# Performance work log

Hardware: AMD Instinct MI355X
Metric: run time of the kernel (lower is better)

Reference implementation:

```python
import jax, jax.numpy as jnp
from jax import lax
import numpy as np

BINS = 25
K = 5  # entropy patch size
EPS = 1e-5


def conv2d(x, w, b, stride, pad):
    y = lax.conv_general_dilated(x, w, (stride, stride), [(pad, pad), (pad, pad)],
                                 dimension_numbers=("NCHW", "OIHW", "NCHW"))
    return y + b[None, :, None, None]


def group_norm_per_channel(x, w, b):
    # GroupNorm with num_groups == num_channels: per-channel norm over H,W (biased var)
    mu = x.mean(axis=(2, 3), keepdims=True)
    v = x.var(axis=(2, 3), keepdims=True)
    return (x - mu) / jnp.sqrt(v + EPS) * w[None, :, None, None] + b[None, :, None, None]


def channel_entropy(x):
    # x: (b,c,h,w). Unfold into 5x5 patches, per-patch histc(bins=25) over patch
    # values using that patch's min/max range (torch.histc default), then entropy.
    b, c, h, w = x.shape
    ho, wo = h - K + 1, w - K + 1
    # (b,c,K*K,L) -- fixed 25-position loop, vectorized over all data dims
    patches = jnp.stack([x[:, :, i:i + ho, j:j + wo]
                         for i in range(K) for j in range(K)], axis=2)
    patches = patches.reshape(b, c, K * K, ho * wo)
    mn = patches.min(axis=2, keepdims=True)
    mx = patches.max(axis=2, keepdims=True)
    rng = jnp.where(mx > mn, mx - mn, jnp.ones_like(mx))
    bins = jnp.clip(jnp.floor((patches - mn) / rng * BINS), 0, BINS - 1).astype(jnp.int32)
    # histogram via comparison one-hot: (b,c,L,BINS)
    counts = (bins[..., None] == jnp.arange(BINS, dtype=jnp.int32)).sum(axis=2)
    pk = counts.astype(x.dtype) / (K * K)
    ent = (-pk * jnp.log(jnp.clip(pk, 1e-5, 1.0 - 1e-5))).sum(axis=-1).mean(axis=-1)  # (b,c)
    return ent[:, :, None, None]


def instance_norm_ent(x, w, b):
    ent = channel_entropy(lax.stop_gradient(x))
    mu = x.mean(axis=(2, 3), keepdims=True)
    n = x.shape[2] * x.shape[3]
    v = x.var(axis=(2, 3), keepdims=True) * (n / (n - 1))  # unbiased var (torch default)
    return (x - mu) / jnp.sqrt(v + EPS) * w[None, :, None, None] * ent + b[None, :, None, None]


def setup_inputs() -> dict:
    key = jax.random.key(0)
    ks = jax.random.split(key, 24)
    s = 0.05
    d = {
        "x": jax.random.normal(ks[0], (64, 3, 224, 224), jnp.float32),
        "conv0_w": jax.random.normal(ks[1], (8, 3, 7, 7), jnp.float32) * s,
        "conv0_b": jax.random.normal(ks[2], (8,), jnp.float32) * s,
        "conv1_w": jax.random.normal(ks[3], (16, 8, 5, 5), jnp.float32) * s,
        "conv1_b": jax.random.normal(ks[4], (16,), jnp.float32) * s,
        "conv2_w": jax.random.normal(ks[5], (32, 16, 3, 3), jnp.float32) * s,
        "conv2_b": jax.random.normal(ks[6], (32,), jnp.float32) * s,
        "gn0_w": jnp.ones((8,), jnp.float32) + jax.random.normal(ks[7], (8,), jnp.float32) * s,
        "gn0_b": jax.random.normal(ks[8], (8,), jnp.float32) * s,
        "n1_w": jnp.ones((16,), jnp.float32) + jax.random.normal(ks[9], (16,), jnp.float32) * s,
        "n1_b": jax.random.normal(ks[10], (16,), jnp.float32) * s,
        "n2_w": jnp.ones((32,), jnp.float32) + jax.random.normal(ks[11], (32,), jnp.float32) * s,
        "n2_b": jax.random.normal(ks[12], (32,), jnp.float32) * s,
        "bn_g": jnp.ones((10368,), jnp.float32) + jax.random.normal(ks[13], (10368,), jnp.float32) * s,
        "bn_b": jax.random.normal(ks[14], (10368,), jnp.float32) * s,
        "fc1_w": jax.random.normal(ks[15], (32, 10368), jnp.float32) * 0.01,
        "fc1_b": jax.random.normal(ks[16], (32,), jnp.float32) * s,
        "shape_w": jax.random.normal(ks[17], (5, 32), jnp.float32) * s,
        "shape_b": jax.random.normal(ks[18], (5,), jnp.float32) * s,
        "vern_w": jax.random.normal(ks[19], (2, 32), jnp.float32) * s,
        "vern_b": jax.random.normal(ks[20], (2,), jnp.float32) * s,
    }
    return d


def reference(x, conv0_w, conv0_b, conv1_w, conv1_b, conv2_w, conv2_b,
              gn0_w, gn0_b, n1_w, n1_b, n2_w, n2_b,
              bn_g, bn_b, fc1_w, fc1_b, shape_w, shape_b, vern_w, vern_b):
    h = conv2d(x, conv0_w, conv0_b, 4, 2)          # (b,8,56,56)
    h = jax.nn.relu(group_norm_per_channel(h, gn0_w, gn0_b))
    h = conv2d(h, conv1_w, conv1_b, 3, 1)          # (b,16,18,18)
    h = jax.nn.relu(instance_norm_ent(h, n1_w, n1_b))
    h = conv2d(h, conv2_w, conv2_b, 1, 1)          # (b,32,18,18)
    h = jax.nn.relu(instance_norm_ent(h, n2_w, n2_b))
    h = h.reshape(h.shape[0], -1)                  # (b,10368)
    # BatchNorm1d (training mode: batch stats, biased var)
    mu = h.mean(axis=0)
    v = h.var(axis=0)
    h = (h - mu) / jnp.sqrt(v + EPS) * bn_g + bn_b
    h = jax.nn.relu(h @ fc1_w.T + fc1_b)           # (b,32)
    out_shape = jax.nn.softmax(h @ shape_w.T + shape_b, axis=-1)
    out_vern = jax.nn.softmax(h @ vern_w.T + vern_b, axis=-1)
    return (out_shape, out_vern)
```

## Files before the change

### kernel.cpp

```cpp
#include <hip/hip_runtime.h>
#include <math.h>

#define EPSD 1e-5


__device__ __forceinline__ double waveReduceSumD(double v) {
#pragma unroll
    for (int off = 32; off > 0; off >>= 1)
        v += __shfl_down(v, off, 64);
    return v;
}

template <int NW>
__device__ __forceinline__ double blockReduceSumD(double v, double* buf) {
    int lane = threadIdx.x & 63;
    int w = threadIdx.x >> 6;
    v = waveReduceSumD(v);
    __syncthreads();
    if (lane == 0) buf[w] = v;
    __syncthreads();
    double tot = 0.0;
#pragma unroll
    for (int i = 0; i < NW; i++) tot += buf[i];
    return tot;
}

__device__ __forceinline__ void build_ent_tab(float* tab) {
    int t = threadIdx.x;
    if (t < 26) {
        if (t == 0) tab[0] = 0.f;
        else {
            double pk = (double)t / 25.0;
            double cl = fmin(fmax(pk, 1e-5), 1.0 - 1e-5);
            tab[t] = (float)(-pk * log(cl));
        }
    }
}

__device__ __forceinline__ float patch_ent(const float* ch, int py, int px, const float* tab) {
    float pv[25];
#pragma unroll
    for (int i = 0; i < 5; i++)
#pragma unroll
        for (int j = 0; j < 5; j++)
            pv[i * 5 + j] = ch[(py + i) * 18 + px + j];
    float mn = pv[0], mx = pv[0];
#pragma unroll
    for (int k = 1; k < 25; k++) { mn = fminf(mn, pv[k]); mx = fmaxf(mx, pv[k]); }
    float rng = (mx > mn) ? (mx - mn) : 1.0f;
    unsigned long long a0 = 0ull, a1 = 0ull;
    int a2 = 0;
#pragma unroll
    for (int k = 0; k < 25; k++) {
        float tt = (pv[k] - mn) / rng * 25.0f;
        int bi = (int)floorf(tt);
        bi = bi < 0 ? 0 : (bi > 24 ? 24 : bi);
        unsigned sh0 = ((unsigned)(5 * bi)) & 63u;
        unsigned sh1 = ((unsigned)(5 * bi - 60)) & 63u;
        a0 += (bi < 12) ? (1ull << sh0) : 0ull;
        a1 += (bi >= 12 && bi < 24) ? (1ull << sh1) : 0ull;
        a2 += (bi == 24) ? 1 : 0;
    }
    float ent = 0.f;
#pragma unroll
    for (int k = 0; k < 12; k++) ent += tab[(a0 >> (5 * k)) & 31ull];
#pragma unroll
    for (int k = 0; k < 12; k++) ent += tab[(a1 >> (5 * k)) & 31ull];
    ent += tab[a2];
    return ent;
}

__global__ __launch_bounds__(256, 4) void k_conv0(const float* __restrict__ x,
                                                  const float* __restrict__ w,
                                                  const float* __restrict__ bias,
                                                  float* __restrict__ h0raw,
                                                  double* __restrict__ part0) {
    __shared__ float wsh[1176];
    __shared__ double redbuf[4][16];
    int tile = blockIdx.x;
    int b = blockIdx.y;
    int t = threadIdx.x;
    for (int i = t; i < 1176; i += 256) {
        int tap = i >> 3, c = i & 7;
        wsh[i] = w[c * 147 + tap];
    }
    __syncthreads();
    const float* xb = x + (size_t)b * 150528;
    float acc[8];
    if (t < 224) {
        int oy = tile * 4 + (t / 56);
        int ox = t % 56;
        int y0 = oy * 4 - 2, x0 = ox * 4 - 2;
#pragma unroll
        for (int c = 0; c < 8; c++) acc[c] = bias[c];
        if (y0 >= 0 && y0 + 6 < 224 && x0 >= 0 && x0 + 6 < 224) {
#pragma unroll 1
            for (int ci = 0; ci < 3; ci++) {
                const float* xp = xb + ci * 50176 + y0 * 224 + x0;
#pragma unroll
                for (int ky = 0; ky < 7; ky++) {
#pragma unroll
                    for (int kx = 0; kx < 7; kx++) {
                        float v = xp[ky * 224 + kx];
                        const float4* wv = (const float4*)&wsh[(ci * 49 + ky * 7 + kx) << 3];
                        float4 wa = wv[0], wb = wv[1];
                        acc[0] += v * wa.x; acc[1] += v * wa.y;
                        acc[2] += v * wa.z; acc[3] += v * wa.w;
                        acc[4] += v * wb.x; acc[5] += v * wb.y;
                        acc[6] += v * wb.z; acc[7] += v * wb.w;
                    }
                }
            }
        } else {
            int ky0 = y0 < 0 ? -y0 : 0;
            int ky1 = (224 - y0) < 7 ? (224 - y0) : 7;
            int kx0 = x0 < 0 ? -x0 : 0;
            int kx1 = (224 - x0) < 7 ? (224 - x0) : 7;
#pragma unroll 1
            for (int ci = 0; ci < 3; ci++) {
                const float* xp = xb + ci * 50176;
                for (int ky = ky0; ky < ky1; ky++) {
                    const float* row = xp + (y0 + ky) * 224 + x0;
                    for (int kx = kx0; kx < kx1; kx++) {
                        float v = row[kx];
                        const float4* wv = (const float4*)&wsh[(ci * 49 + ky * 7 + kx) << 3];
                        float4 wa = wv[0], wb = wv[1];
                        acc[0] += v * wa.x; acc[1] += v * wa.y;
                        acc[2] += v * wa.z; acc[3] += v * wa.w;
                        acc[4] += v * wb.x; acc[5] += v * wb.y;
                        acc[6] += v * wb.z; acc[7] += v * wb.w;
                    }
                }
            }
        }
        int opix = oy * 56 + ox;
#pragma unroll
        for (int c = 0; c < 8; c++)
            h0raw[((size_t)b * 8 + c) * 3136 + opix] = acc[c];
    } else {
#pragma unroll
        for (int c = 0; c < 8; c++) acc[c] = 0.f;
    }
    int wv = t >> 6, lane = t & 63;
#pragma unroll
    for (int c = 0; c < 8; c++) {
        double rs = waveReduceSumD((double)acc[c]);
        double rq = waveReduceSumD((double)acc[c] * (double)acc[c]);
        if (lane == 0) { redbuf[wv][c * 2] = rs; redbuf[wv][c * 2 + 1] = rq; }
    }
    __syncthreads();
    if (t < 16) {
        double tot = redbuf[0][t] + redbuf[1][t] + redbuf[2][t] + redbuf[3][t];
        part0[(((size_t)b * 14 + tile) << 4) + t] = tot;
    }
}

__global__ __launch_bounds__(1024) void k_conv1_ent(const float* __restrict__ h0raw,
                                                    const double* __restrict__ part0,
                                                    const float* __restrict__ gw,
                                                    const float* __restrict__ gb,
                                                    const float* __restrict__ w,
                                                    const float* __restrict__ bias,
                                                    const float* __restrict__ nw,
                                                    const float* __restrict__ nb,
                                                    float* __restrict__ h1) {
    __shared__ float xin[25088];
    __shared__ float wsh[800];
    __shared__ float vals[1296];
    __shared__ float tab[26];
    __shared__ float gnp[16];
    __shared__ double redbuf[16][2];
    __shared__ double entbuf[16];
    __shared__ float prm[4][3];
    int b = blockIdx.x >> 2;
    int grp = blockIdx.x & 3;
    int t = threadIdx.x;
    if (t < 8) {
        double s = 0.0, s2 = 0.0;
        const double* p = part0 + ((size_t)b * 14) * 16;
        for (int tile = 0; tile < 14; tile++) {
            s += p[tile * 16 + t * 2];
            s2 += p[tile * 16 + t * 2 + 1];
        }
        double mean = s / 3136.0;
        double var = s2 / 3136.0 - mean * mean;
        double rstd = 1.0 / sqrt(var + EPSD);
        double sc = (double)gw[t] * rstd;
        gnp[t] = (float)sc;
        gnp[8 + t] = (float)((double)gb[t] - mean * sc);
    }
    for (int i = t; i < 800; i += 1024) wsh[i] = w[grp * 800 + i];
    build_ent_tab(tab);
    __syncthreads();
    for (int i = t; i < 25088; i += 1024) {
        int ci = i / 3136;
        xin[i] = fmaxf(h0raw[(size_t)b * 25088 + i] * gnp[ci] + gnp[8 + ci], 0.f);
    }
    __syncthreads();

    int wv = t >> 6, lane = t & 63;
    int c = wv >> 2;
    int q = wv & 3;
    const float* wp0 = wsh + c * 200;
    float* vch = vals + c * 324;
    float bv = bias[grp * 4 + c];
    double s = 0.0, s2 = 0.0;
    for (int p = q * 81 + lane; p < q * 81 + 81; p += 64) {
        int oy = p / 18, ox = p % 18;
        int y0 = oy * 3 - 1, x0 = ox * 3 - 1;
        float acc = bv;
        if (oy >= 1 && ox >= 1) {
#pragma unroll 1
            for (int ci = 0; ci < 8; ci++) {
                const float* xp = xin + ci * 3136 + y0 * 56 + x0;
                const float* wp = wp0 + ci * 25;
#pragma unroll
                for (int ky = 0; ky < 5; ky++)
#pragma unroll
                    for (int kx = 0; kx < 5; kx++)
                        acc += xp[ky * 56 + kx] * wp[ky * 5 + kx];
            }
        } else {
            int ky0 = y0 < 0 ? 1 : 0;
            int kx0 = x0 < 0 ? 1 : 0;
            for (int ci = 0; ci < 8; ci++) {
                const float* xp = xin + ci * 3136;
                const float* wp = wp0 + ci * 25;
                for (int ky = ky0; ky < 5; ky++) {
                    const float* row = xp + (y0 + ky) * 56 + x0;
                    for (int kx = kx0; kx < 5; kx++)
                        acc += row[kx] * wp[ky * 5 + kx];
                }
            }
        }
        vch[p] = acc;
        s += (double)acc; s2 += (double)acc * (double)acc;
    }
    s = waveReduceSumD(s);
    s2 = waveReduceSumD(s2);
    if (lane == 0) { redbuf[wv][0] = s; redbuf[wv][1] = s2; }
    __syncthreads();
    double ent = 0.0;
    if (lane < 49) {
        int pi = q * 49 + lane;
        ent = (double)patch_ent(vch, pi / 14, pi % 14, tab);
    }
    ent = waveReduceSumD(ent);
    if (lane == 0) entbuf[wv] = ent;
    __syncthreads();
    if (t < 4) {
        double ss = 0.0, qq = 0.0, ee = 0.0;
        for (int k = 0; k < 4; k++) {
            ss += redbuf[t * 4 + k][0];
            qq += redbuf[t * 4 + k][1];
            ee += entbuf[t * 4 + k];
        }
        double entmean = ee / 196.0;
        double mean = ss / 324.0;
        double varb = qq / 324.0 - mean * mean;
        double varu = varb * (324.0 / 323.0);
        double rstd = 1.0 / sqrt(varu + EPSD);
        prm[t][0] = (float)mean;
        prm[t][1] = (float)((double)nw[grp * 4 + t] * entmean * rstd);
        prm[t][2] = nb[grp * 4 + t];
    }
    __syncthreads();
    float* outp = h1 + ((size_t)b * 16 + grp * 4) * 324;
    for (int i = t; i < 1296; i += 1024) {
        int cc = i / 324;
        outp[i] = fmaxf((vals[i] - prm[cc][0]) * prm[cc][1] + prm[cc][2], 0.f);
    }
}

__global__ __launch_bounds__(256) void k_conv2_ent(const float* __restrict__ in,
                                                   const float* __restrict__ w,
                                                   const float* __restrict__ bias,
                                                   const float* __restrict__ nw,
                                                   const float* __restrict__ nb,
                                                   float* __restrict__ out) {
    __shared__ float xin[5184];
    __shared__ float vals[324];
    __shared__ float wsh[144];
    __shared__ float tab[26];
    __shared__ double rbuf[4];
    int b = blockIdx.x >> 5;
    int c = blockIdx.x & 31;
    int t = threadIdx.x;
    const float* xb = in + (size_t)b * 5184;
    for (int i = t; i < 5184; i += 256) xin[i] = xb[i];
    for (int i = t; i < 144; i += 256) wsh[i] = w[c * 144 + i];
    build_ent_tab(tab);
    __syncthreads();
    float bv = bias[c];
    double s = 0.0, s2 = 0.0;
    {
        int oy = 1 + (t >> 4), ox = 1 + (t & 15);
        const float* base = xin + (oy - 1) * 18 + (ox - 1);
        float acc = bv;
        for (int ci = 0; ci < 16; ci++) {
            const float* xp = base + ci * 324;
            const float* wp = wsh + ci * 9;
#pragma unroll
            for (int ky = 0; ky < 3; ky++)
#pragma unroll
                for (int kx = 0; kx < 3; kx++)
                    acc += xp[ky * 18 + kx] * wp[ky * 3 + kx];
        }
        vals[oy * 18 + ox] = acc;
        s += (double)acc; s2 += (double)acc * (double)acc;
    }
    if (t < 68) {
        int oy, ox;
        if (t < 18)      { oy = 0;      ox = t; }
        else if (t < 36) { oy = 17;     ox = t - 18; }
        else if (t < 52) { oy = t - 35; ox = 0; }
        else             { oy = t - 51; ox = 17; }
        int y0 = oy - 1, x0 = ox - 1;
        int ky0 = y0 < 0 ? 1 : 0;
        int ky1 = (18 - y0) < 3 ? 2 : 3;
        int kx0 = x0 < 0 ? 1 : 0;
        int kx1 = (18 - x0) < 3 ? 2 : 3;
        float acc = bv;
        for (int ci = 0; ci < 16; ci++) {
            const float* xp = xin + ci * 324;
            const float* wp = wsh + ci * 9;
            for (int ky = ky0; ky < ky1; ky++) {
                const float* row = xp + (y0 + ky) * 18 + x0;
                for (int kx = kx0; kx < kx1; kx++)
                    acc += row[kx] * wp[ky * 3 + kx];
            }
        }
        vals[oy * 18 + ox] = acc;
        s += (double)acc; s2 += (double)acc * (double)acc;
    }
    __syncthreads();
    double ent = 0.0;
    if (t < 196) ent = (double)patch_ent(vals, t / 14, t % 14, tab);
    double entmean = blockReduceSumD<4>(ent, rbuf) / 196.0;
    double ssum  = blockReduceSumD<4>(s, rbuf);
    double s2sum = blockReduceSumD<4>(s2, rbuf);
    double mean = ssum / 324.0;
    double varb = s2sum / 324.0 - mean * mean;
    double varu = varb * (324.0 / 323.0);
    double rstd = 1.0 / sqrt(varu + EPSD);
    float sc = (float)((double)nw[c] * entmean * rstd);
    float mu = (float)mean;
    float be = nb[c];
    float* outp = out + ((size_t)b * 32 + c) * 324;
    for (int idx = t; idx < 324; idx += 256)
        outp[idx] = fmaxf((vals[idx] - mu) * sc + be, 0.f);
}

__global__ __launch_bounds__(256) void k_bnstats(const float* __restrict__ h2,
                                                 const float* __restrict__ g,
                                                 const float* __restrict__ bb,
                                                 float* __restrict__ scale,
                                                 float* __restrict__ shift) {
    int f = blockIdx.x * 256 + threadIdx.x;
    if (f >= 10368) return;
    double s = 0.0, s2 = 0.0;
    for (int b = 0; b < 64; b++) {
        double v = (double)h2[(size_t)b * 10368 + f];
        s += v; s2 += v * v;
    }
    double mean = s / 64.0;
    double var = s2 / 64.0 - mean * mean;
    double rstd = 1.0 / sqrt(var + EPSD);
    double sc = (double)g[f] * rstd;
    scale[f] = (float)sc;
    shift[f] = (float)((double)bb[f] - mean * sc);
}

__global__ __launch_bounds__(256) void k_fc1(const float* __restrict__ h2,
                                             const float* __restrict__ scale,
                                             const float* __restrict__ shift,
                                             const float* __restrict__ w1,
                                             const float* __restrict__ b1,
                                             float* __restrict__ fcout) {
    __shared__ double rbuf[4];
    int b = blockIdx.x >> 5;
    int j = blockIdx.x & 31;
    const float* hb = h2 + (size_t)b * 10368;
    const float* wj = w1 + (size_t)j * 10368;
    double acc = 0.0;
    for (int f = threadIdx.x; f < 10368; f += 256)
        acc += (double)((hb[f] * scale[f] + shift[f]) * wj[f]);
    acc = blockReduceSumD<4>(acc, rbuf);
    if (threadIdx.x == 0)
        fcout[b * 32 + j] = (float)fmax(acc + (double)b1[j], 0.0);
}

__global__ __launch_bounds__(64) void k_heads(const float* __restrict__ fc,
                                              const float* __restrict__ sw,
                                              const float* __restrict__ sb,
                                              const float* __restrict__ vw,
                                              const float* __restrict__ vb,
                                              float* __restrict__ out) {
    int b = threadIdx.x;
    double h[32];
#pragma unroll
    for (int i = 0; i < 32; i++) h[i] = (double)fc[b * 32 + i];
    double lg[5];
    double mx = -1e300;
#pragma unroll
    for (int k = 0; k < 5; k++) {
        double a = (double)sb[k];
#pragma unroll
        for (int i = 0; i < 32; i++) a += h[i] * (double)sw[k * 32 + i];
        lg[k] = a;
        mx = fmax(mx, a);
    }
    double se = 0.0;
#pragma unroll
    for (int k = 0; k < 5; k++) { lg[k] = exp(lg[k] - mx); se += lg[k]; }
#pragma unroll
    for (int k = 0; k < 5; k++) out[b * 5 + k] = (float)(lg[k] / se);
    double l0 = (double)vb[0], l1 = (double)vb[1];
#pragma unroll
    for (int i = 0; i < 32; i++) { l0 += h[i] * (double)vw[i]; l1 += h[i] * (double)vw[32 + i]; }
    double m = fmax(l0, l1);
    double e0 = exp(l0 - m), e1 = exp(l1 - m);
    double inv = 1.0 / (e0 + e1);
    out[320 + b * 2 + 0] = (float)(e0 * inv);
    out[320 + b * 2 + 1] = (float)(e1 * inv);
}

extern "C" void kernel_launch(void* const* d_in, const int* in_sizes, int n_in,
                              void* d_out, int out_size, void* d_ws, size_t ws_size,
                              hipStream_t stream) {
    const float* x       = (const float*)d_in[0];
    const float* conv0_w = (const float*)d_in[1];
    const float* conv0_b = (const float*)d_in[2];
    const float* conv1_w = (const float*)d_in[3];
    const float* conv1_b = (const float*)d_in[4];
    const float* conv2_w = (const float*)d_in[5];
    const float* conv2_b = (const float*)d_in[6];
    const float* gn0_w   = (const float*)d_in[7];
    const float* gn0_b   = (const float*)d_in[8];
    const float* n1_w    = (const float*)d_in[9];
    const float* n1_b    = (const float*)d_in[10];
    const float* n2_w    = (const float*)d_in[11];
    const float* n2_b    = (const float*)d_in[12];
    const float* bn_g    = (const float*)d_in[13];
    const float* bn_b    = (const float*)d_in[14];
    const float* fc1_w   = (const float*)d_in[15];
    const float* fc1_b   = (const float*)d_in[16];
    const float* shape_w = (const float*)d_in[17];
    const float* shape_b = (const float*)d_in[18];
    const float* vern_w  = (const float*)d_in[19];
    const float* vern_b  = (const float*)d_in[20];
    float* out = (float*)d_out;

    double* part0 = (double*)d_ws;
    float* fbase   = (float*)(part0 + 14336);
    float* h0raw   = fbase;
    float* h1      = h0raw + 1605632;
    float* h2      = h1 + 331776;
    float* bnscale = h2 + 663552;
    float* bnshift = bnscale + 10368;
    float* fc      = bnshift + 10368;

    k_conv0<<<dim3(14, 64), dim3(256), 0, stream>>>(x, conv0_w, conv0_b, h0raw, part0);
    k_conv1_ent<<<dim3(256), dim3(1024), 0, stream>>>(h0raw, part0, gn0_w, gn0_b,
                                                      conv1_w, conv1_b, n1_w, n1_b, h1);
    k_conv2_ent<<<dim3(2048), dim3(256), 0, stream>>>(h1, conv2_w, conv2_b, n2_w, n2_b, h2);
    k_bnstats<<<dim3(41), dim3(256), 0, stream>>>(h2, bn_g, bn_b, bnscale, bnshift);
    k_fc1<<<dim3(2048), dim3(256), 0, stream>>>(h2, bnscale, bnshift, fc1_w, fc1_b, fc);
    k_heads<<<dim3(1), dim3(64), 0, stream>>>(fc, shape_w, shape_b, vern_w, vern_b, out);
}
```

Before: 258.0 us.

## Stage conv0 input in phase-split LDS tile, read weights as uniform scalars, split bnstats

conv0 now loads a zero-padded 19-row input tile into shared memory with float4 global loads, de-interleaved by x mod 4 so stride-4 taps read contiguous LDS. Its weights come straight from global memory at wave-uniform addresses so they can go through scalar loads. conv1 interleaves channel pairs in LDS for float2 reads and likewise drops the weight staging, and conv2 reads its weights from global memory. bnstats splits the batch reduction over four waves across 162 blocks to use more CUs. The costs are more LDS per conv0 block, lower declared occupancy, and reliance on the compiler emitting scalar weight loads.

```diff
diff --git a/kernel.cpp b/kernel.cpp
--- a/kernel.cpp
+++ b/kernel.cpp
@@ -70,76 +70,61 @@
     return ent;
 }
 
-__global__ __launch_bounds__(256, 4) void k_conv0(const float* __restrict__ x,
+__global__ __launch_bounds__(256, 3) void k_conv0(const float* __restrict__ x,
                                                   const float* __restrict__ w,
                                                   const float* __restrict__ bias,
                                                   float* __restrict__ h0raw,
                                                   double* __restrict__ part0) {
-    __shared__ float wsh[1176];
+    __shared__ float tile[12996];
     __shared__ double redbuf[4][16];
-    int tile = blockIdx.x;
+    int tl = blockIdx.x;
     int b = blockIdx.y;
     int t = threadIdx.x;
-    for (int i = t; i < 1176; i += 256) {
-        int tap = i >> 3, c = i & 7;
-        wsh[i] = w[c * 147 + tap];
-    }
-    __syncthreads();
+    for (int i = t; i < 12996; i += 256) tile[i] = 0.f;
+    __syncthreads();
+    int y_base = tl * 16 - 2;
     const float* xb = x + (size_t)b * 150528;
+    for (int i = t; i < 3192; i += 256) {
+        int rowid = i / 56, f4 = i % 56;
+        int ci = rowid / 19, r = rowid % 19;
+        int yIn = y_base + r;
+        if (yIn >= 0 && yIn < 224) {
+            float4 v = *(const float4*)&xb[ci * 50176 + yIn * 224 + f4 * 4];
+            float* tp = tile + ci * 4332 + r * 228;
+            tp[114 + f4] = v.x;
+            tp[171 + f4] = v.y;
+            tp[f4 + 1]   = v.z;
+            tp[58 + f4]  = v.w;
+        }
+    }
+    __syncthreads();
     float acc[8];
+#pragma unroll
+    for (int c = 0; c < 8; c++) acc[c] = 0.f;
     if (t < 224) {
-        int oy = tile * 4 + (t / 56);
+        int ry = t / 56;
         int ox = t % 56;
-        int y0 = oy * 4 - 2, x0 = ox * 4 - 2;
 #pragma unroll
         for (int c = 0; c < 8; c++) acc[c] = bias[c];
-        if (y0 >= 0 && y0 + 6 < 224 && x0 >= 0 && x0 + 6 < 224) {
-#pragma unroll 1
-            for (int ci = 0; ci < 3; ci++) {
-                const float* xp = xb + ci * 50176 + y0 * 224 + x0;
-#pragma unroll
-                for (int ky = 0; ky < 7; ky++) {
-#pragma unroll
-                    for (int kx = 0; kx < 7; kx++) {
-                        float v = xp[ky * 224 + kx];
-                        const float4* wv = (const float4*)&wsh[(ci * 49 + ky * 7 + kx) << 3];
-                        float4 wa = wv[0], wb = wv[1];
-                        acc[0] += v * wa.x; acc[1] += v * wa.y;
-                        acc[2] += v * wa.z; acc[3] += v * wa.w;
-                        acc[4] += v * wb.x; acc[5] += v * wb.y;
-                        acc[6] += v * wb.z; acc[7] += v * wb.w;
-                    }
+#pragma unroll
+        for (int ci = 0; ci < 3; ci++) {
+#pragma unroll
+            for (int ky = 0; ky < 7; ky++) {
+                const float* rp = tile + ci * 4332 + (4 * ry + ky) * 228;
+#pragma unroll
+                for (int kx = 0; kx < 7; kx++) {
+                    float v = rp[(kx & 3) * 57 + ox + (kx >> 2)];
+#pragma unroll
+                    for (int c = 0; c < 8; c++)
+                        acc[c] += v * w[c * 147 + ci * 49 + ky * 7 + kx];
                 }
             }
-        } else {
-            int ky0 = y0 < 0 ? -y0 : 0;
-            int ky1 = (224 - y0) < 7 ? (224 - y0) : 7;
-            int kx0 = x0 < 0 ? -x0 : 0;
-            int kx1 = (224 - x0) < 7 ? (224 - x0) : 7;
-#pragma unroll 1
-            for (int ci = 0; ci < 3; ci++) {
-                const float* xp = xb + ci * 50176;
-                for (int ky = ky0; ky < ky1; ky++) {
-                    const float* row = xp + (y0 + ky) * 224 + x0;
-                    for (int kx = kx0; kx < kx1; kx++) {
-                        float v = row[kx];
-                        const float4* wv = (const float4*)&wsh[(ci * 49 + ky * 7 + kx) << 3];
-                        float4 wa = wv[0], wb = wv[1];
-                        acc[0] += v * wa.x; acc[1] += v * wa.y;
-                        acc[2] += v * wa.z; acc[3] += v * wa.w;
-                        acc[4] += v * wb.x; acc[5] += v * wb.y;
-                        acc[6] += v * wb.z; acc[7] += v * wb.w;
-                    }
-                }
-            }
-        }
+        }
+        int oy = tl * 4 + ry;
         int opix = oy * 56 + ox;
 #pragma unroll
         for (int c = 0; c < 8; c++)
             h0raw[((size_t)b * 8 + c) * 3136 + opix] = acc[c];
-    } else {
-#pragma unroll
-        for (int c = 0; c < 8; c++) acc[c] = 0.f;
     }
     int wv = t >> 6, lane = t & 63;
 #pragma unroll
@@ -151,7 +136,7 @@
     __syncthreads();
     if (t < 16) {
         double tot = redbuf[0][t] + redbuf[1][t] + redbuf[2][t] + redbuf[3][t];
-        part0[(((size_t)b * 14 + tile) << 4) + t] = tot;
+        part0[(((size_t)b * 14 + tl) << 4) + t] = tot;
     }
 }
 
@@ -164,8 +149,7 @@
                                                     const float* __restrict__ nw,
                                                     const float* __restrict__ nb,
                                                     float* __restrict__ h1) {
-    __shared__ float xin[25088];
-    __shared__ float wsh[800];
+    __shared__ float xin2[25088];
     __shared__ float vals[1296];
     __shared__ float tab[26];
     __shared__ float gnp[16];
@@ -189,47 +173,53 @@
         gnp[t] = (float)sc;
         gnp[8 + t] = (float)((double)gb[t] - mean * sc);
     }
-    for (int i = t; i < 800; i += 1024) wsh[i] = w[grp * 800 + i];
     build_ent_tab(tab);
     __syncthreads();
     for (int i = t; i < 25088; i += 1024) {
-        int ci = i / 3136;
-        xin[i] = fmaxf(h0raw[(size_t)b * 25088 + i] * gnp[ci] + gnp[8 + ci], 0.f);
+        int ci = i / 3136, px = i - ci * 3136;
+        float v = fmaxf(h0raw[(size_t)b * 25088 + i] * gnp[ci] + gnp[8 + ci], 0.f);
+        xin2[(ci >> 1) * 6272 + px * 2 + (ci & 1)] = v;
     }
     __syncthreads();
 
     int wv = t >> 6, lane = t & 63;
     int c = wv >> 2;
     int q = wv & 3;
-    const float* wp0 = wsh + c * 200;
+    int j_u = __builtin_amdgcn_readfirstlane(grp * 4 + c);
+    const float* wg = w + (size_t)j_u * 200;
     float* vch = vals + c * 324;
-    float bv = bias[grp * 4 + c];
+    float bv = bias[j_u];
     double s = 0.0, s2 = 0.0;
     for (int p = q * 81 + lane; p < q * 81 + 81; p += 64) {
-        int oy = p / 18, ox = p % 18;
+        int oy = p / 18, ox = p - oy * 18;
         int y0 = oy * 3 - 1, x0 = ox * 3 - 1;
         float acc = bv;
         if (oy >= 1 && ox >= 1) {
-#pragma unroll 1
-            for (int ci = 0; ci < 8; ci++) {
-                const float* xp = xin + ci * 3136 + y0 * 56 + x0;
-                const float* wp = wp0 + ci * 25;
+#pragma unroll
+            for (int c2 = 0; c2 < 4; c2++) {
+                const float* xp = xin2 + c2 * 6272 + (y0 * 56 + x0) * 2;
+                const float* wp0 = wg + (2 * c2) * 25;
 #pragma unroll
                 for (int ky = 0; ky < 5; ky++)
 #pragma unroll
-                    for (int kx = 0; kx < 5; kx++)
-                        acc += xp[ky * 56 + kx] * wp[ky * 5 + kx];
+                    for (int kx = 0; kx < 5; kx++) {
+                        float2 v = *(const float2*)&xp[(ky * 56 + kx) * 2];
+                        acc += v.x * wp0[ky * 5 + kx];
+                        acc += v.y * wp0[25 + ky * 5 + kx];
+                    }
             }
         } else {
             int ky0 = y0 < 0 ? 1 : 0;
             int kx0 = x0 < 0 ? 1 : 0;
-            for (int ci = 0; ci < 8; ci++) {
-                const float* xp = xin + ci * 3136;
-                const float* wp = wp0 + ci * 25;
+            for (int c2 = 0; c2 < 4; c2++) {
+                const float* xp = xin2 + c2 * 6272;
+                const float* wp0 = wg + (2 * c2) * 25;
                 for (int ky = ky0; ky < 5; ky++) {
-                    const float* row = xp + (y0 + ky) * 56 + x0;
-                    for (int kx = kx0; kx < 5; kx++)
-                        acc += row[kx] * wp[ky * 5 + kx];
+                    for (int kx = kx0; kx < 5; kx++) {
+                        float2 v = *(const float2*)&xp[((y0 + ky) * 56 + x0 + kx) * 2];
+                        acc += v.x * wp0[ky * 5 + kx];
+                        acc += v.y * wp0[25 + ky * 5 + kx];
+                    }
                 }
             }
         }
@@ -280,7 +270,6 @@
                                                    float* __restrict__ out) {
     __shared__ float xin[5184];
     __shared__ float vals[324];
-    __shared__ float wsh[144];
     __shared__ float tab[26];
     __shared__ double rbuf[4];
     int b = blockIdx.x >> 5;
@@ -288,18 +277,19 @@
     int t = threadIdx.x;
     const float* xb = in + (size_t)b * 5184;
     for (int i = t; i < 5184; i += 256) xin[i] = xb[i];
-    for (int i = t; i < 144; i += 256) wsh[i] = w[c * 144 + i];
     build_ent_tab(tab);
     __syncthreads();
+    const float* wc = w + c * 144;
     float bv = bias[c];
     double s = 0.0, s2 = 0.0;
     {
         int oy = 1 + (t >> 4), ox = 1 + (t & 15);
         const float* base = xin + (oy - 1) * 18 + (ox - 1);
         float acc = bv;
+#pragma unroll
         for (int ci = 0; ci < 16; ci++) {
             const float* xp = base + ci * 324;
-            const float* wp = wsh + ci * 9;
+            const float* wp = wc + ci * 9;
 #pragma unroll
             for (int ky = 0; ky < 3; ky++)
 #pragma unroll
@@ -323,7 +313,7 @@
         float acc = bv;
         for (int ci = 0; ci < 16; ci++) {
             const float* xp = xin + ci * 324;
-            const float* wp = wsh + ci * 9;
+            const float* wp = wc + ci * 9;
             for (int ky = ky0; ky < ky1; ky++) {
                 const float* row = xp + (y0 + ky) * 18 + x0;
                 for (int kx = kx0; kx < kx1; kx++)
@@ -356,19 +346,27 @@
                                                  const float* __restrict__ bb,
                                                  float* __restrict__ scale,
                                                  float* __restrict__ shift) {
-    int f = blockIdx.x * 256 + threadIdx.x;
-    if (f >= 10368) return;
+    __shared__ double sb[4][64], qb[4][64];
+    int lane = threadIdx.x & 63;
+    int q = threadIdx.x >> 6;
+    int f = blockIdx.x * 64 + lane;
     double s = 0.0, s2 = 0.0;
-    for (int b = 0; b < 64; b++) {
+    for (int b = q * 16; b < q * 16 + 16; b++) {
         double v = (double)h2[(size_t)b * 10368 + f];
         s += v; s2 += v * v;
     }
-    double mean = s / 64.0;
-    double var = s2 / 64.0 - mean * mean;
-    double rstd = 1.0 / sqrt(var + EPSD);
-    double sc = (double)g[f] * rstd;
-    scale[f] = (float)sc;
-    shift[f] = (float)((double)bb[f] - mean * sc);
+    sb[q][lane] = s; qb[q][lane] = s2;
+    __syncthreads();
+    if (threadIdx.x < 64) {
+        double S = sb[0][lane] + sb[1][lane] + sb[2][lane] + sb[3][lane];
+        double Q = qb[0][lane] + qb[1][lane] + qb[2][lane] + qb[3][lane];
+        double mean = S / 64.0;
+        double var = Q / 64.0 - mean * mean;
+        double rstd = 1.0 / sqrt(var + EPSD);
+        double sc = (double)g[f] * rstd;
+        scale[f] = (float)sc;
+        shift[f] = (float)((double)bb[f] - mean * sc);
+    }
 }
 
 __global__ __launch_bounds__(256) void k_fc1(const float* __restrict__ h2,
@@ -464,7 +462,7 @@
     k_conv1_ent<<<dim3(256), dim3(1024), 0, stream>>>(h0raw, part0, gn0_w, gn0_b,
                                                       conv1_w, conv1_b, n1_w, n1_b, h1);
     k_conv2_ent<<<dim3(2048), dim3(256), 0, stream>>>(h1, conv2_w, conv2_b, n2_w, n2_b, h2);
-    k_bnstats<<<dim3(41), dim3(256), 0, stream>>>(h2, bn_g, bn_b, bnscale, bnshift);
+    k_bnstats<<<dim3(162), dim3(256), 0, stream>>>(h2, bn_g, bn_b, bnscale, bnshift);
     k_fc1<<<dim3(2048), dim3(256), 0, stream>>>(h2, bnscale, bnshift, fc1_w, fc1_b, fc);
     k_heads<<<dim3(1), dim3(64), 0, stream>>>(fc, shape_w, shape_b, vern_w, vern_b, out);
 }
```

Measured after the change: 249.2 us. -3.4%, faster.
